# Performance work log

Hardware: AMD Instinct MI355X
Metric: run time of the kernel (lower is better)

Reference implementation:

```python
import jax, jax.numpy as jnp
import numpy as np

MARGIN = 0.3
EPS = 1e-12

def setup_inputs() -> dict:
    key = jax.random.key(0)
    k1, k2 = jax.random.split(key)
    B, D, NUM_IDS = 1024, 2048, 256
    features = jax.random.normal(k1, (B, D), dtype=jnp.float32)
    labels = jax.random.randint(k2, (B,), 0, NUM_IDS, dtype=jnp.int64)
    return {"features": features, "labels": labels}

def _pairwise_euclidean(features):
    # dist^2 = |x_i|^2 + |x_j|^2 - 2 x_i . x_j, clamped then sqrt (as in torch ref)
    sq = jnp.sum(features * features, axis=1)  # [B]
    d2 = sq[:, None] + sq[None, :] - 2.0 * (features @ features.T)
    return jnp.sqrt(jnp.maximum(d2, EPS))

def reference(features, labels):
    B = features.shape[0]
    dist = _pairwise_euclidean(features)  # [B, B]
    eq = labels[None, :] == labels[:, None]  # [B, B]; eq[i] == labels_equal row i
    eye = jnp.eye(B, dtype=bool)
    pos_mask = eq & ~eye
    neg_mask = ~eq
    neg_inf = jnp.float32(-jnp.inf)
    pos_inf = jnp.float32(jnp.inf)
    hardest_pos = jnp.max(jnp.where(pos_mask, dist, neg_inf), axis=1)  # [B]
    hardest_neg = jnp.min(jnp.where(neg_mask, dist, pos_inf), axis=1)  # [B]
    valid = jnp.any(pos_mask, axis=1) & jnp.any(neg_mask, axis=1)  # rows contributing a triplet
    per_row = jax.nn.relu(hardest_pos - hardest_neg + MARGIN)
    per_row = jnp.where(valid, per_row, 0.0)
    n_valid = jnp.sum(valid)
    loss = jnp.sum(per_row) / jnp.maximum(n_valid, 1).astype(per_row.dtype)
    num_active = jnp.sum(valid & (per_row > 0))
    return loss, num_active
```

## Files before the change

### kernel.cpp

```cpp
#include <hip/hip_runtime.h>
#include <math.h>

#define B_SZ 1024
#define D_SZ 2048
#define MARGIN 0.3f

typedef _Float16 f16x8 __attribute__((ext_vector_type(8)));
typedef float f32x16 __attribute__((ext_vector_type(16)));

union FragU { uint4 u; f16x8 v; };
union H4 { _Float16 h[4]; uint2 u; };

#define AS1 __attribute__((address_space(1)))
#define AS3 __attribute__((address_space(3)))



__global__ __launch_bounds__(256) void prep_kernel(const float* __restrict__ F,
                                                   _Float16* __restrict__ Fh,
                                                   float* __restrict__ sqpart,
                                                   int* __restrict__ hp,
                                                   int* __restrict__ hn,
                                                   int* __restrict__ flags) {
    __shared__ _Float16 slab[64][136];
    __shared__ float part[64];

    const int b = blockIdx.x;
    const int i = b >> 4;
    const int kseg = b & 15;
    const int t = threadIdx.x;
    const int lane = t & 63;
    const int w = t >> 6;

    const int idx = b * 256 + t;
    if (idx < 1024) {
        hp[idx] = 0;
        hn[idx] = 0x7F800000;
        flags[idx] = 0;
    }

#pragma unroll
    for (int q = 0; q < 8; ++q) {
        const int rl = q * 8 + (t >> 5);
        const int c4 = (t & 31) * 4;
        const float4 v = *(const float4*)(F + (size_t)(i * 64 + rl) * D_SZ +
                                          kseg * 128 + c4);
        float s = v.x * v.x + v.y * v.y + v.z * v.z + v.w * v.w;
#pragma unroll
        for (int mask = 1; mask < 32; mask <<= 1) s += __shfl_xor(s, mask);
        if ((t & 31) == 0) part[rl] = s;
        H4 p;
        p.h[0] = (_Float16)v.x; p.h[1] = (_Float16)v.y;
        p.h[2] = (_Float16)v.z; p.h[3] = (_Float16)v.w;
        *(uint2*)&slab[rl][c4] = p.u;
    }
    __syncthreads();

    if (t < 64) sqpart[kseg * 1024 + i * 64 + t] = part[t];

#pragma unroll
    for (int q2 = 0; q2 < 4; ++q2) {
        const int u = w * 4 + q2;
        const int kb = u >> 1;
        const int rg = u & 1;
        const uint4 d = *(const uint4*)&slab[rg * 32 + (lane & 31)]
                                          [kb * 16 + (lane >> 5) * 8];
        const size_t g = (size_t)((i * 128 + kseg * 8 + kb) * 2 + rg);
        *(uint4*)((char*)Fh + g * 1024 + (size_t)lane * 16) = d;
    }
}


#define SUB_SZ 3072
#define WAVE_STAGE (6 * SUB_SZ)

__global__ __launch_bounds__(256) void dist_f16_kernel(
    const _Float16* __restrict__ Fh, const int* __restrict__ labels,
    const float* __restrict__ sqpart, int* __restrict__ hp,
    int* __restrict__ hn, int* __restrict__ flags) {
    __shared__ __align__(16) char stage[4 * WAVE_STAGE];
    __shared__ int labR[64], labC[32];
    __shared__ float sqR[64], sqC[32];

    const int t = threadIdx.x;
    const int lane = t & 63;
    const int w = t >> 6;

    const int xcd = blockIdx.x & 7;
    const int cidx = blockIdx.x >> 3;
    const int bi = (xcd >> 1) * 4 + (cidx >> 4);
    const int bj = (xcd & 1) * 16 + (cidx & 15);
    const int rowBase = bi * 64, colBase = bj * 32;

    if (t < 64) {
        const int row = rowBase + t;
        float s = 0.f;
#pragma unroll
        for (int p = 0; p < 16; ++p) s += sqpart[p * 1024 + row];
        sqR[t] = s;
        labR[t] = labels[row];
    } else if (t < 96) {
        const int e = t - 64;
        const int row = colBase + e;
        float s = 0.f;
#pragma unroll
        for (int p = 0; p < 16; ++p) s += sqpart[p * 1024 + row];
        sqC[e] = s;
        labC[e] = labels[row];
    }
    __syncthreads();
    asm volatile("s_waitcnt vmcnt(0)" ::: "memory");

    const char* __restrict__ FhB = (const char*)Fh;
    char* wbase = stage + w * WAVE_STAGE;
    const char* rbase = wbase + lane * 16;

    f32x16 acc[2];
#pragma unroll
    for (int a = 0; a < 2; ++a)
#pragma unroll
        for (int e = 0; e < 16; ++e) acc[a][e] = 0.f;

    auto ISSUE = [&](int s, int b) {
        const int kb16 = w * 32 + s;
        const size_t aOff = (size_t)((bi * 128 + kb16) * 2) * 1024 + (size_t)lane * 16;
        const size_t bOff = (size_t)(((bj >> 1) * 128 + kb16) * 2 + (bj & 1)) * 1024 +
                            (size_t)lane * 16;
        char* dA = wbase + b * SUB_SZ;
        __builtin_amdgcn_global_load_lds((const AS1 void*)(FhB + aOff),
                                         (AS3 void*)(dA), 16, 0, 0);
        __builtin_amdgcn_global_load_lds((const AS1 void*)(FhB + aOff + 1024),
                                         (AS3 void*)(dA + 1024), 16, 0, 0);
        __builtin_amdgcn_global_load_lds((const AS1 void*)(FhB + bOff),
                                         (AS3 void*)(dA + 2048), 16, 0, 0);
    };
    auto COMPUTE = [&](int b) {
        const char* rb = rbase + b * SUB_SZ;
        FragU a0, a1, v0;
        a0.u = *(const uint4*)(rb);
        a1.u = *(const uint4*)(rb + 1024);
        v0.u = *(const uint4*)(rb + 2048);
        acc[0] = __builtin_amdgcn_mfma_f32_32x32x16_f16(a0.v, v0.v, acc[0], 0, 0, 0);
        acc[1] = __builtin_amdgcn_mfma_f32_32x32x16_f16(a1.v, v0.v, acc[1], 0, 0, 0);
    };

#define WAITN(n) asm volatile("s_waitcnt vmcnt(" #n ")" ::: "memory"); __builtin_amdgcn_sched_barrier(0)

    ISSUE(0, 0); ISSUE(1, 1); ISSUE(2, 2); ISSUE(3, 3); ISSUE(4, 4);
    for (int s6 = 0; s6 < 24; s6 += 6) {
        ISSUE(s6 + 5, 5);  WAITN(15); COMPUTE(0);
        ISSUE(s6 + 6, 0);  WAITN(15); COMPUTE(1);
        ISSUE(s6 + 7, 1);  WAITN(15); COMPUTE(2);
        ISSUE(s6 + 8, 2);  WAITN(15); COMPUTE(3);
        ISSUE(s6 + 9, 3);  WAITN(15); COMPUTE(4);
        ISSUE(s6 + 10, 4); WAITN(15); COMPUTE(5);
    }
    ISSUE(29, 5); WAITN(15); COMPUTE(0);
    ISSUE(30, 0); WAITN(15); COMPUTE(1);
    ISSUE(31, 1); WAITN(15); COMPUTE(2);
    WAITN(12); COMPUTE(3);
    WAITN(9);  COMPUTE(4);
    WAITN(6);  COMPUTE(5);
    WAITN(3);  COMPUTE(0);
    WAITN(0);  COMPUTE(1);

#undef WAITN

    __syncthreads();

    char* cb = stage;
#pragma unroll
    for (int fr = 0; fr < 2; ++fr)
#pragma unroll
        for (int g = 0; g < 4; ++g) {
            float4 v;
            v.x = acc[fr][g * 4 + 0];
            v.y = acc[fr][g * 4 + 1];
            v.z = acc[fr][g * 4 + 2];
            v.w = acc[fr][g * 4 + 3];
            *(float4*)(cb + (size_t)(w * 8192) +
                       (size_t)((fr * 4 + g) * 64 + lane) * 16) = v;
        }
    __syncthreads();

    if (w < 2) {
        const int fr = w;
        float cS[16];
#pragma unroll
        for (int e = 0; e < 16; ++e) cS[e] = 0.f;
#pragma unroll
        for (int wp = 0; wp < 4; ++wp)
#pragma unroll
            for (int g = 0; g < 4; ++g) {
                float4 v = *(const float4*)(cb + (size_t)(wp * 8192) +
                                            (size_t)((fr * 4 + g) * 64 + lane) * 16);
                cS[g * 4 + 0] += v.x;
                cS[g * 4 + 1] += v.y;
                cS[g * 4 + 2] += v.z;
                cS[g * 4 + 3] += v.w;
            }

        const float BIG = 1e38f;
        const int h = lane >> 5;
        const int colL = lane & 31;
        const int j = colBase + colL;
        const int lj = labC[colL];
        const float sqj = sqC[colL];
#pragma unroll
        for (int k = 0; k < 16; ++k) {
            const int rowL = fr * 32 + (k & 3) + 8 * (k >> 2) + 4 * h;
            const int i = rowBase + rowL;
            const float d2 = sqR[rowL] + sqj - 2.f * cS[k];
            const float d = sqrtf(fmaxf(d2, 1e-12f));
            const bool eq = (labR[rowL] == lj);
            const bool isPos = eq && (i != j);
            float pv = isPos ? d : -BIG;
            float nv = eq ? BIG : d;
            int pf = (isPos ? 1 : 0) | (eq ? 0 : 2);
#pragma unroll
            for (int mask = 1; mask < 32; mask <<= 1) {
                pv = fmaxf(pv, __shfl_xor(pv, mask));
                nv = fminf(nv, __shfl_xor(nv, mask));
                pf |= __shfl_xor(pf, mask);
            }
            if (colL == 0) {
                if (pf & 1) atomicMax(&hp[i], __float_as_int(pv));
                if (pf & 2) atomicMin(&hn[i], __float_as_int(nv));
                if (pf) atomicOr(&flags[i], pf);
            }
        }
    }
}


__global__ __launch_bounds__(1024) void final_kernel(const int* __restrict__ hp,
                                                     const int* __restrict__ hn,
                                                     const int* __restrict__ flags,
                                                     float* __restrict__ out) {
    __shared__ float ssum[16];
    __shared__ int svalid[16], sact[16];
    const int t = threadIdx.x;
    const float hpv = __int_as_float(hp[t]);
    const float hnv = __int_as_float(hn[t]);
    const int f = flags[t];
    const bool valid = (f == 3);
    float pr = fmaxf(hpv - hnv + MARGIN, 0.f);
    if (!valid) pr = 0.f;
    int act = (valid && pr > 0.f) ? 1 : 0;
    int vld = valid ? 1 : 0;
    float s = pr;
    for (int off = 32; off; off >>= 1) {
        s += __shfl_down(s, off);
        act += __shfl_down(act, off);
        vld += __shfl_down(vld, off);
    }
    if ((t & 63) == 0) {
        ssum[t >> 6] = s;
        svalid[t >> 6] = vld;
        sact[t >> 6] = act;
    }
    __syncthreads();
    if (t == 0) {
        float tot = 0.f;
        int nv = 0, na = 0;
#pragma unroll
        for (int i = 0; i < 16; ++i) {
            tot += ssum[i];
            nv += svalid[i];
            na += sact[i];
        }
        out[0] = tot / (float)(nv > 1 ? nv : 1);
        out[1] = (float)na;
    }
}


#define BM 64
#define BN 64
#define BK 32

__global__ __launch_bounds__(256) void sq_kernel(const float* __restrict__ F,
                                                 float* __restrict__ sq) {
    int row = blockIdx.x;
    const float4* r4 = (const float4*)(F + (size_t)row * D_SZ);
    int t = threadIdx.x;
    float s = 0.f;
#pragma unroll
    for (int q = 0; q < 2; ++q) {
        float4 v = r4[t + q * 256];
        s += v.x * v.x + v.y * v.y + v.z * v.z + v.w * v.w;
    }
    for (int off = 32; off; off >>= 1) s += __shfl_down(s, off);
    __shared__ float wsum[4];
    if ((t & 63) == 0) wsum[t >> 6] = s;
    __syncthreads();
    if (t == 0) sq[row] = wsum[0] + wsum[1] + wsum[2] + wsum[3];
}

__global__ __launch_bounds__(256) void init_kernel(int* __restrict__ hp,
                                                   int* __restrict__ hn,
                                                   int* __restrict__ flags) {
    int i = blockIdx.x * 256 + threadIdx.x;
    hp[i] = 0;
    hn[i] = 0x7F800000;
    flags[i] = 0;
}

__global__ __launch_bounds__(256) void dist_f32_kernel(
    const float* __restrict__ F, const int* __restrict__ labels,
    const float* __restrict__ sq, int* __restrict__ hp, int* __restrict__ hn,
    int* __restrict__ flags) {
    __shared__ float As[BK][BM];
    __shared__ float Bs[BK][BN];
    __shared__ int labR[BM], labC[BN];
    __shared__ float sqR[BM], sqC[BN];

    const int rowBase = blockIdx.y * BM;
    const int colBase = blockIdx.x * BN;
    const int t = threadIdx.x;
    const int tx = t & 15;
    const int ty = t >> 4;

    if (t < 64) {
        labR[t] = labels[rowBase + t];
        sqR[t] = sq[rowBase + t];
    } else if (t < 128) {
        int u = t - 64;
        labC[u] = labels[colBase + u];
        sqC[u] = sq[colBase + u];
    }

    float acc[4][4] = {{0.f}};
    const int m = t & 63;
    const int q = t >> 6;
    const float* aRow = F + (size_t)(rowBase + m) * D_SZ + q * 8;
    const float* bRow = F + (size_t)(colBase + m) * D_SZ + q * 8;

    for (int k0 = 0; k0 < D_SZ; k0 += BK) {
        float4 a0 = *(const float4*)(aRow + k0);
        float4 a1 = *(const float4*)(aRow + k0 + 4);
        float4 b0 = *(const float4*)(bRow + k0);
        float4 b1 = *(const float4*)(bRow + k0 + 4);
        __syncthreads();
        int kb = q * 8;
        As[kb + 0][m] = a0.x; As[kb + 1][m] = a0.y;
        As[kb + 2][m] = a0.z; As[kb + 3][m] = a0.w;
        As[kb + 4][m] = a1.x; As[kb + 5][m] = a1.y;
        As[kb + 6][m] = a1.z; As[kb + 7][m] = a1.w;
        Bs[kb + 0][m] = b0.x; Bs[kb + 1][m] = b0.y;
        Bs[kb + 2][m] = b0.z; Bs[kb + 3][m] = b0.w;
        Bs[kb + 4][m] = b1.x; Bs[kb + 5][m] = b1.y;
        Bs[kb + 6][m] = b1.z; Bs[kb + 7][m] = b1.w;
        __syncthreads();
#pragma unroll
        for (int kk = 0; kk < BK; ++kk) {
            float4 a = *(const float4*)&As[kk][ty * 4];
            float4 b = *(const float4*)&Bs[kk][tx * 4];
            acc[0][0] += a.x * b.x; acc[0][1] += a.x * b.y;
            acc[0][2] += a.x * b.z; acc[0][3] += a.x * b.w;
            acc[1][0] += a.y * b.x; acc[1][1] += a.y * b.y;
            acc[1][2] += a.y * b.z; acc[1][3] += a.y * b.w;
            acc[2][0] += a.z * b.x; acc[2][1] += a.z * b.y;
            acc[2][2] += a.z * b.z; acc[2][3] += a.z * b.w;
            acc[3][0] += a.w * b.x; acc[3][1] += a.w * b.y;
            acc[3][2] += a.w * b.z; acc[3][3] += a.w * b.w;
        }
    }

    float mp[4], mn[4];
    int pf[4];
#pragma unroll
    for (int rr = 0; rr < 4; ++rr) {
        const int i = rowBase + ty * 4 + rr;
        const int li = labR[ty * 4 + rr];
        const float si = sqR[ty * 4 + rr];
        mp[rr] = -3.4e38f;
        mn[rr] = 3.4e38f;
        pf[rr] = 0;
#pragma unroll
        for (int c = 0; c < 4; ++c) {
            const int j = colBase + tx * 4 + c;
            const float d2 = si + sqC[tx * 4 + c] - 2.f * acc[rr][c];
            const float dist = sqrtf(fmaxf(d2, 1e-12f));
            const bool eq = (li == labC[tx * 4 + c]);
            if (eq && (i != j)) {
                mp[rr] = fmaxf(mp[rr], dist);
                pf[rr] |= 1;
            }
            if (!eq) {
                mn[rr] = fminf(mn[rr], dist);
                pf[rr] |= 2;
            }
        }
    }
#pragma unroll
    for (int mask = 1; mask < 16; mask <<= 1)
#pragma unroll
        for (int rr = 0; rr < 4; ++rr) {
            mp[rr] = fmaxf(mp[rr], __shfl_xor(mp[rr], mask));
            mn[rr] = fminf(mn[rr], __shfl_xor(mn[rr], mask));
            pf[rr] |= __shfl_xor(pf[rr], mask);
        }
    if (tx == 0) {
#pragma unroll
        for (int rr = 0; rr < 4; ++rr) {
            const int i = rowBase + ty * 4 + rr;
            if (pf[rr] & 1) atomicMax(&hp[i], __float_as_int(mp[rr]));
            if (pf[rr] & 2) atomicMin(&hn[i], __float_as_int(mn[rr]));
            if (pf[rr]) atomicOr(&flags[i], pf[rr]);
        }
    }
}


extern "C" void kernel_launch(void* const* d_in, const int* in_sizes, int n_in,
                              void* d_out, int out_size, void* d_ws, size_t ws_size,
                              hipStream_t stream) {
    const float* F = (const float*)d_in[0];
    const int* labels = (const int*)d_in[1];
    float* out = (float*)d_out;
    char* ws = (char*)d_ws;

    const size_t FH = (size_t)B_SZ * D_SZ * 2;
    const size_t SQP = 16 * 1024 * sizeof(float);
    const size_t need = FH + SQP + 12 * 1024;

    if (ws_size >= need) {
        _Float16* Fh = (_Float16*)ws;
        float* sqpart = (float*)(ws + FH);
        char* tail = ws + FH + SQP;
        int* hp = (int*)tail;
        int* hn = (int*)(tail + 4096);
        int* flags = (int*)(tail + 8192);

        prep_kernel<<<256, 256, 0, stream>>>(F, Fh, sqpart, hp, hn, flags);
        dist_f16_kernel<<<512, 256, 0, stream>>>(Fh, labels, sqpart, hp, hn, flags);
        final_kernel<<<1, 1024, 0, stream>>>(hp, hn, flags, out);
    } else {
        float* sq = (float*)ws;
        int* hp = (int*)(ws + 4096);
        int* hn = (int*)(ws + 8192);
        int* flags = (int*)(ws + 12288);

        sq_kernel<<<B_SZ, 256, 0, stream>>>(F, sq);
        init_kernel<<<B_SZ / 256, 256, 0, stream>>>(hp, hn, flags);
        dim3 grid(B_SZ / BN, B_SZ / BM);
        dist_f32_kernel<<<grid, 256, 0, stream>>>(F, labels, sq, hp, hn, flags);
        final_kernel<<<1, 1024, 0, stream>>>(hp, hn, flags, out);
    }
}
```

Baseline: 32.48 us.

## Replace LDS-staged async load pipeline with direct register double-buffered loads

The six-deep global_load_lds staging ring with explicit vmcnt waits is replaced by loading MFMA fragments straight from global memory into registers, double-buffered across two register sets. Shared memory shrinks from a large per-wave staging area to a 32KB epilogue buffer, and launch bounds request two blocks per CU so occupancy can hide latency. The cost is a shallower prefetch depth (one step ahead) that relies on the compiler's scheduling and on occupancy instead of explicit deep pipelining.

Result: no change. 32.28 us (-0.6%).

```diff
diff --git a/kernel.cpp b/kernel.cpp
--- a/kernel.cpp
+++ b/kernel.cpp
@@ -10,9 +10,6 @@
 
 union FragU { uint4 u; f16x8 v; };
 union H4 { _Float16 h[4]; uint2 u; };
-
-#define AS1 __attribute__((address_space(1)))
-#define AS3 __attribute__((address_space(3)))
 
 
 
@@ -71,14 +68,11 @@
 }
 
 
-#define SUB_SZ 3072
-#define WAVE_STAGE (6 * SUB_SZ)
-
-__global__ __launch_bounds__(256) void dist_f16_kernel(
+__global__ __launch_bounds__(256, 2) void dist_f16_kernel(
     const _Float16* __restrict__ Fh, const int* __restrict__ labels,
     const float* __restrict__ sqpart, int* __restrict__ hp,
     int* __restrict__ hn, int* __restrict__ flags) {
-    __shared__ __align__(16) char stage[4 * WAVE_STAGE];
+    __shared__ __align__(16) char cb[32768];
     __shared__ int labR[64], labC[32];
     __shared__ float sqR[64], sqC[32];
 
@@ -109,11 +103,11 @@
         labC[e] = labels[row];
     }
     __syncthreads();
-    asm volatile("s_waitcnt vmcnt(0)" ::: "memory");
 
     const char* __restrict__ FhB = (const char*)Fh;
-    char* wbase = stage + w * WAVE_STAGE;
-    const char* rbase = wbase + lane * 16;
+    const char* pA0 = FhB + (size_t)((bi * 128 + w * 32) * 2) * 1024 + (size_t)lane * 16;
+    const char* pB0 = FhB + (size_t)(((bj >> 1) * 128 + w * 32) * 2 + (bj & 1)) * 1024 +
+                      (size_t)lane * 16;
 
     f32x16 acc[2];
 #pragma unroll
@@ -121,54 +115,33 @@
 #pragma unroll
         for (int e = 0; e < 16; ++e) acc[a][e] = 0.f;
 
-    auto ISSUE = [&](int s, int b) {
-        const int kb16 = w * 32 + s;
-        const size_t aOff = (size_t)((bi * 128 + kb16) * 2) * 1024 + (size_t)lane * 16;
-        const size_t bOff = (size_t)(((bj >> 1) * 128 + kb16) * 2 + (bj & 1)) * 1024 +
-                            (size_t)lane * 16;
-        char* dA = wbase + b * SUB_SZ;
-        __builtin_amdgcn_global_load_lds((const AS1 void*)(FhB + aOff),
-                                         (AS3 void*)(dA), 16, 0, 0);
-        __builtin_amdgcn_global_load_lds((const AS1 void*)(FhB + aOff + 1024),
-                                         (AS3 void*)(dA + 1024), 16, 0, 0);
-        __builtin_amdgcn_global_load_lds((const AS1 void*)(FhB + bOff),
-                                         (AS3 void*)(dA + 2048), 16, 0, 0);
+    auto LOADREG = [&](int s, uint4* r) {
+        const size_t off = (size_t)s * 2048;
+        r[0] = *(const uint4*)(pA0 + off);
+        r[1] = *(const uint4*)(pA0 + off + 1024);
+        r[2] = *(const uint4*)(pB0 + off);
     };
-    auto COMPUTE = [&](int b) {
-        const char* rb = rbase + b * SUB_SZ;
+    auto MFMA2 = [&](const uint4* r) {
         FragU a0, a1, v0;
-        a0.u = *(const uint4*)(rb);
-        a1.u = *(const uint4*)(rb + 1024);
-        v0.u = *(const uint4*)(rb + 2048);
+        a0.u = r[0];
+        a1.u = r[1];
+        v0.u = r[2];
         acc[0] = __builtin_amdgcn_mfma_f32_32x32x16_f16(a0.v, v0.v, acc[0], 0, 0, 0);
         acc[1] = __builtin_amdgcn_mfma_f32_32x32x16_f16(a1.v, v0.v, acc[1], 0, 0, 0);
     };
 
-#define WAITN(n) asm volatile("s_waitcnt vmcnt(" #n ")" ::: "memory"); __builtin_amdgcn_sched_barrier(0)
-
-    ISSUE(0, 0); ISSUE(1, 1); ISSUE(2, 2); ISSUE(3, 3); ISSUE(4, 4);
-    for (int s6 = 0; s6 < 24; s6 += 6) {
-        ISSUE(s6 + 5, 5);  WAITN(15); COMPUTE(0);
-        ISSUE(s6 + 6, 0);  WAITN(15); COMPUTE(1);
-        ISSUE(s6 + 7, 1);  WAITN(15); COMPUTE(2);
-        ISSUE(s6 + 8, 2);  WAITN(15); COMPUTE(3);
-        ISSUE(s6 + 9, 3);  WAITN(15); COMPUTE(4);
-        ISSUE(s6 + 10, 4); WAITN(15); COMPUTE(5);
-    }
-    ISSUE(29, 5); WAITN(15); COMPUTE(0);
-    ISSUE(30, 0); WAITN(15); COMPUTE(1);
-    ISSUE(31, 1); WAITN(15); COMPUTE(2);
-    WAITN(12); COMPUTE(3);
-    WAITN(9);  COMPUTE(4);
-    WAITN(6);  COMPUTE(5);
-    WAITN(3);  COMPUTE(0);
-    WAITN(0);  COMPUTE(1);
-
-#undef WAITN
-
-    __syncthreads();
-
-    char* cb = stage;
+    uint4 ra[3], rb[3];
+    LOADREG(0, ra);
+#pragma unroll
+    for (int s = 0; s < 32; s += 2) {
+        LOADREG(s + 1, rb);
+        MFMA2(ra);
+        if (s + 2 < 32) LOADREG(s + 2, ra);
+        MFMA2(rb);
+    }
+
+    __syncthreads();
+
 #pragma unroll
     for (int fr = 0; fr < 2; ++fr)
 #pragma unroll
```
